# Kernel optimization log

Hardware: AMD Instinct MI355X
Metric: run time of the kernel (lower is better)

The kernel has to match this reference:

```python
import jax, jax.numpy as jnp
import numpy as np

DIM = 1024
HEADS = 16
DIM_HEAD = 64
INNER = HEADS * DIM_HEAD  # 1024
SCALE = 1.0 / DIM_HEAD ** 0.5


def setup_inputs() -> dict:
    key = jax.random.key(0)
    ks = jax.random.split(key, 5)
    x = jax.random.normal(ks[0], (4, 2048, DIM), dtype=jnp.float32)
    # nn.Linear weights stored as [out, in]; we keep [in, out] for x @ W
    Wq = jax.random.normal(ks[1], (DIM, INNER), dtype=jnp.float32) * (1.0 / np.sqrt(DIM))
    Wkv = jax.random.normal(ks[2], (DIM, 2 * INNER), dtype=jnp.float32) * (1.0 / np.sqrt(DIM))
    Wo = jax.random.normal(ks[3], (INNER, DIM), dtype=jnp.float32) * (1.0 / np.sqrt(INNER))
    bo = jax.random.normal(ks[4], (DIM,), dtype=jnp.float32) * 0.01
    return {"x": x, "Wq": Wq, "Wkv": Wkv, "Wo": Wo, "bo": bo}


def reference(x, Wq, Wkv, Wo, bo):
    b, n, _ = x.shape
    q = x @ Wq                      # [b, n, inner]
    kv = x @ Wkv                    # [b, n, 2*inner]
    k, v = jnp.split(kv, 2, axis=2)
    # 'b n (h d) -> b h n d'
    q = q.reshape(b, n, HEADS, DIM_HEAD).transpose(0, 2, 1, 3)
    k = k.reshape(b, n, HEADS, DIM_HEAD).transpose(0, 2, 1, 3)
    v = v.reshape(b, n, HEADS, DIM_HEAD).transpose(0, 2, 1, 3)
    scores = jnp.einsum('bhid,bhjd->bhij', q, k) * SCALE  # [b,h,n,n]
    attn = jax.nn.softmax(scores, axis=-1)
    out = jnp.einsum('bhij,bhjd->bhid', attn, v)          # [b,h,n,d]
    out = out.transpose(0, 2, 1, 3).reshape(b, n, INNER)  # 'b h n d -> b n (h d)'
    return out @ Wo + bo
```

## Files before the change

### kernel.cpp

```cpp
#include <hip/hip_runtime.h>
#include <hip/hip_bf16.h>

typedef unsigned short u16;
typedef unsigned int u32;
typedef __attribute__((ext_vector_type(8))) short s8v;
typedef __attribute__((ext_vector_type(4))) float f4v;
typedef __attribute__((ext_vector_type(4))) unsigned short u16x4;
typedef __attribute__((ext_vector_type(4))) unsigned int u32x4;

#define MFMA16(a,b,c) __builtin_amdgcn_mfma_f32_16x16x32_bf16((a),(b),(c),0,0,0)

#define TOKENS 8192
#define SEQ    2048
#define NH     16
#define DH     64
#define DIMK   1024
#define QPRE   0.18033688f

#if defined(__has_builtin)
#if __has_builtin(__builtin_amdgcn_exp2f)
#define EXP2(x) __builtin_amdgcn_exp2f(x)
#else
#define EXP2(x) __expf((x) * 0.69314718f)
#endif
#else
#define EXP2(x) __expf((x) * 0.69314718f)
#endif

__device__ __forceinline__ u16 f2bf(float x){
  union { float f; u32 u; } v; v.f = x;
  u32 r = v.u + 0x7FFFu + ((v.u >> 16) & 1u);
  return (u16)(r >> 16);
}

__device__ __forceinline__ void gld16(const u16* g, u16* s){
  __builtin_amdgcn_global_load_lds(
      (const __attribute__((address_space(1))) unsigned int*)(const void*)g,
      (__attribute__((address_space(3))) unsigned int*)(void*)s,
      16, 0, 0);
}

__global__ __launch_bounds__(256) void k_cast(const float* __restrict__ src,
                                              u16* __restrict__ dst){
  int i = (blockIdx.x * 256 + threadIdx.x) * 4;
  float4 v = *(const float4*)(src + i);
  u16x4 vh;
  float a[4] = {v.x, v.y, v.z, v.w};
#pragma unroll
  for (int j = 0; j < 4; j++) vh[j] = f2bf(a[j]);
  *(u16x4*)(dst + i) = vh;
}

__global__ __launch_bounds__(256) void k_transpose(const float* __restrict__ s0, int c0,
                                                   const float* __restrict__ s1, int c1,
                                                   int K, u16* __restrict__ dh){
  __shared__ float tile[64][65];
  int nb = blockIdx.x * 64, kb = blockIdx.y * 64;
  int tr = threadIdx.x >> 6, tc = threadIdx.x & 63;
#pragma unroll
  for (int i = 0; i < 16; i++){
    int k = kb + tr + i * 4, n = nb + tc;
    float v = (n < c0) ? s0[(size_t)k * c0 + n] : s1[(size_t)k * c1 + (n - c0)];
    tile[tr + i * 4][tc] = v;
  }
  __syncthreads();
#pragma unroll
  for (int i = 0; i < 16; i++){
    int nl = tr + i * 4, kl = tc;
    dh[(size_t)(nb + nl) * K + (kb + kl)] = f2bf(tile[kl][nl]);
  }
}

#define GQ_STAGE_A(buf,h,t) do{ \
  gld16(As + (size_t)(h)*131072 + (size_t)(t)*64,      &lds[(buf)*32768 + (h)*8192 + w*512]); \
  gld16(As + (size_t)(h)*131072 + (size_t)(t)*64 + 32, &lds[(buf)*32768 + (h)*8192 + 4096 + w*512]); }while(0)
#define GQ_STAGE_B(buf,h,t) do{ \
  gld16(Bs + (size_t)(h)*131072 + (size_t)(t)*64,      &lds[(buf)*32768 + 16384 + (h)*8192 + w*512]); \
  gld16(Bs + (size_t)(h)*131072 + (size_t)(t)*64 + 32, &lds[(buf)*32768 + 16384 + (h)*8192 + 4096 + w*512]); }while(0)
#define GQ_RDA(dst,buf,mh) do{ _Pragma("unroll") for (int i_ = 0; i_ < 4; i_++){ \
  dst[i_][0] = *(const s8v*)&lds[(buf)*32768 + aRB + ((mh)*4+i_)*512]; \
  dst[i_][1] = *(const s8v*)&lds[(buf)*32768 + aRB + 4096 + ((mh)*4+i_)*512]; } }while(0)
#define GQ_RDB(dst,buf,nh) do{ _Pragma("unroll") for (int j_ = 0; j_ < 2; j_++){ \
  dst[j_][0] = *(const s8v*)&lds[(buf)*32768 + bRB + ((nh)*2+j_)*512]; \
  dst[j_][1] = *(const s8v*)&lds[(buf)*32768 + bRB + 4096 + ((nh)*2+j_)*512]; } }while(0)
#define GQ_MMA(aS,bS,mh,nh) do{ __builtin_amdgcn_s_setprio(1); \
  _Pragma("unroll") for (int i_ = 0; i_ < 4; i_++) \
  _Pragma("unroll") for (int j_ = 0; j_ < 2; j_++){ \
    acc[(mh)*4+i_][(nh)*2+j_] = MFMA16(aS[i_][0], bS[j_][0], acc[(mh)*4+i_][(nh)*2+j_]); \
    acc[(mh)*4+i_][(nh)*2+j_] = MFMA16(aS[i_][1], bS[j_][1], acc[(mh)*4+i_][(nh)*2+j_]); } \
  __builtin_amdgcn_s_setprio(0); }while(0)
#define GQ_BAR() do{ asm volatile("" ::: "memory"); __builtin_amdgcn_s_barrier(); asm volatile("" ::: "memory"); }while(0)
#define GQ_VMW2() asm volatile("s_waitcnt vmcnt(2)" ::: "memory")

__global__ __launch_bounds__(512, 2) void k_gemm_qkv(
    const u16* __restrict__ A, const u16* __restrict__ B,
    u16* __restrict__ Qh, u16* __restrict__ Kh, u16* __restrict__ Vth)
{
  __shared__ u16 lds[65536];
  const int tid = threadIdx.x;
  const int w = tid >> 6, lane = tid & 63;
  const int lm = lane & 15, quad = lane >> 4;
  const int wm = w >> 2, wn = w & 3;

  const int bid = blockIdx.x;
  const int xcd = bid & 7, slot = bid >> 3;
  const int nt = slot >> 2;
  const int mloc = slot & 3;
  const int m0 = (xcd * 4 + mloc) * 256, n0 = nt * 256;

  const int srow = lane >> 2;
  const int scol = ((lane & 3) ^ (((lane >> 5) & 1) << 1)) * 8;
  const u16* As = A + (size_t)(m0 + w * 16 + srow) * DIMK + scol;
  const u16* Bs = B + (size_t)(n0 + w * 16 + srow) * DIMK + scol;

  const int swz = (lm & 8) << 1;
  const int aRB = wm * 8192 + lm * 32 + ((quad * 8) ^ swz);
  const int bRB = 16384 + (wn >> 1) * 8192 + (wn & 1) * 2048 + lm * 32 + ((quad * 8) ^ swz);

  f4v acc[8][4];
#pragma unroll
  for (int i = 0; i < 8; i++)
#pragma unroll
    for (int j = 0; j < 4; j++) acc[i][j] = (f4v){0.f, 0.f, 0.f, 0.f};

  s8v aA[4][2], aB[4][2], bA[2][2], bB[2][2];

  GQ_STAGE_A(0,0,0); GQ_STAGE_A(0,1,0); GQ_STAGE_B(0,0,0); GQ_STAGE_B(0,1,0);
  GQ_STAGE_A(1,0,1);
  GQ_VMW2(); GQ_BAR();
  GQ_RDA(aA,0,0); GQ_RDB(bA,0,0);

  for (int it = 0; it < 8; it++){
    const int t1 = 2 * it + 1;
    const int t2 = (it < 7) ? 2 * it + 2 : 15;
    const int t3 = (it < 7) ? 2 * it + 3 : 15;
    GQ_STAGE_A(1,1,t1); GQ_BAR(); GQ_RDA(aB,0,1);                 GQ_MMA(aA,bA,0,0);
    GQ_STAGE_B(1,0,t1); GQ_BAR(); GQ_RDB(bB,0,1);                 GQ_MMA(aB,bA,1,0);
    GQ_STAGE_B(1,1,t1); GQ_BAR();                                 GQ_MMA(aB,bB,1,1);
    GQ_STAGE_A(0,0,t2); GQ_VMW2(); GQ_BAR();
                                  GQ_RDA(aB,1,0); GQ_RDB(bA,1,0); GQ_MMA(aA,bB,0,1);
    GQ_STAGE_A(0,1,t2); GQ_BAR(); GQ_RDA(aA,1,1);                 GQ_MMA(aB,bA,0,0);
    GQ_STAGE_B(0,0,t2); GQ_BAR(); GQ_RDB(bB,1,1);                 GQ_MMA(aA,bA,1,0);
    GQ_STAGE_B(0,1,t2); GQ_BAR();                                 GQ_MMA(aA,bB,1,1);
    GQ_STAGE_A(1,0,t3); GQ_VMW2(); GQ_BAR();
                                  GQ_RDA(aA,0,0); GQ_RDB(bA,0,0); GQ_MMA(aB,bB,0,1);
  }

  if (nt < 8){
#pragma unroll
    for (int ig = 0; ig < 8; ig++)
#pragma unroll
      for (int jg = 0; jg < 4; jg++){
        const int gn = n0 + wn * 64 + jg * 16 + lm;
#pragma unroll
        for (int r = 0; r < 4; r++){
          const int gm = m0 + wm * 128 + ig * 16 + quad * 4 + r;
          float v = acc[ig][jg][r];
          if (gn < 1024){
            Qh[(size_t)gm * DIMK + gn] = f2bf(v * QPRE);
          } else {
            Kh[(size_t)gm * DIMK + (gn - 1024)] = f2bf(v);
          }
        }
      }
  } else {
    __syncthreads();
    u32* bnc = (u32*)lds;
#pragma unroll
    for (int igp = 0; igp < 4; igp++)
#pragma unroll
      for (int jg = 0; jg < 4; jg++){
        const int ddl = wn * 64 + jg * 16 + lm;
        const int colb = wm * 64 + igp * 16 + quad * 4;
        u32x4 p;
#pragma unroll
        for (int r = 0; r < 4; r++)
          p[r] = ((u32)f2bf(acc[2 * igp + 1][jg][r]) << 16) | (u32)f2bf(acc[2 * igp][jg][r]);
        const int col = colb ^ ((lm & 7) << 2);
        *(u32x4*)&bnc[ddl * 128 + col] = p;
      }
    __syncthreads();
    const int row = tid >> 1, half = tid & 1;
    const int df = n0 - 2048 + row;
    const int hh = df >> 6, dd = df & 63;
    const int bbat = m0 >> 11, ii0 = m0 & 2047;
    u32* Vg = (u32*)(Vth + ((size_t)(bbat * NH + hh) * DH + dd) * SEQ + ii0);
#pragma unroll
    for (int c = 0; c < 16; c++){
      const int cc = half * 16 + c;
      const int cb = (cc * 4) ^ ((row & 7) << 2);
      u32x4 q = *(const u32x4*)&bnc[row * 128 + cb];
      *(u32x4*)&Vg[cc * 4] = q;
    }
  }
}

__global__ __launch_bounds__(256) void k_gemm_op(
    const u16* __restrict__ A, const u16* __restrict__ B,
    const float* __restrict__ bias, float* __restrict__ Cf)
{
  __shared__ u16 sA[2][128*32], sB[2][128*32];
  const int tid = threadIdx.x, wave = tid >> 6, lane = tid & 63;
  const int lm = lane & 15, quad = lane >> 4;

  const int bid = blockIdx.x;
  const int xcd = bid & 7, slot = bid >> 3;
  const int nt = slot >> 3, mloc = slot & 7;
  const int m0 = (xcd * 8 + mloc) * 128, n0 = nt * 128;

  const int cof = (lane & 3) * 8;
  const int rsub = lane >> 2;

  f4v acc[4][4];
#pragma unroll
  for (int i = 0; i < 4; i++)
#pragma unroll
    for (int j = 0; j < 4; j++) acc[i][j] = (f4v){0.f, 0.f, 0.f, 0.f};

  const int wm = (wave >> 1) * 64, wn = (wave & 1) * 64;

  for (int kc = 0; kc < 16; kc++){
    int k = kc * 64;
#pragma unroll
    for (int cc = 0; cc < 2; cc++)
#pragma unroll
      for (int half = 0; half < 2; half++){
        int rb = wave * 32 + half * 16;
        gld16(A + (size_t)(m0 + rb + rsub) * DIMK + k + cc * 32 + cof, &sA[cc][rb * 32]);
        gld16(B + (size_t)(n0 + rb + rsub) * DIMK + k + cc * 32 + cof, &sB[cc][rb * 32]);
      }
    __syncthreads();

#pragma unroll
    for (int cc = 0; cc < 2; cc++){
      s8v ah[4], bh[4];
#pragma unroll
      for (int i = 0; i < 4; i++){
        ah[i] = *(const s8v*)&sA[cc][(wm + i * 16 + lm) * 32 + quad * 8];
        bh[i] = *(const s8v*)&sB[cc][(wn + i * 16 + lm) * 32 + quad * 8];
      }
#pragma unroll
      for (int i = 0; i < 4; i++)
#pragma unroll
        for (int j = 0; j < 4; j++)
          acc[i][j] = MFMA16(ah[i], bh[j], acc[i][j]);
    }
    __syncthreads();
  }

#pragma unroll
  for (int i = 0; i < 4; i++)
#pragma unroll
    for (int j = 0; j < 4; j++){
      int gn = n0 + wn + j * 16 + lm;
      float bv = bias[gn];
#pragma unroll
      for (int r = 0; r < 4; r++){
        int gm = m0 + wm + i * 16 + quad * 4 + r;
        Cf[(size_t)gm * DIMK + gn] = acc[i][j][r] + bv;
      }
    }
}

__global__ __launch_bounds__(256, 2) void k_attn(
    const u16* __restrict__ Qh, const u16* __restrict__ Kh, const u16* __restrict__ Vth,
    u16* __restrict__ Oh)
{
  __shared__ u16 sK[2*4096];
  __shared__ u16 sV[2*4096];
  __shared__ u16 sP[16384];
  u32* sPd = (u32*)sP;

  const int bid = blockIdx.x;
  const int xcd = bid & 7, slot = bid >> 3;
  const int g = xcd * 8 + (slot >> 3);
  const int qt = slot & 7;
  const int b = g >> 4, h = g & 15;

  const int tid = threadIdx.x, wave = tid >> 6, lane = tid & 63;
  const int lm = lane & 15, quad = lane >> 4;
  const int tok0 = b * SEQ + qt * 256;
  const int rsub = lane >> 2;
  const int scof = ((lane & 3) ^ (((lane >> 5) & 1) << 1)) * 8;
  const int rsw = (lm & 8) << 1;
  const int psw = (quad & 2) << 2;
  const int plm = (lm & 0xA) | ((lm & 1) << 2) | ((lm >> 2) & 1);

  s8v qf[2][4];
#pragma unroll
  for (int c = 0; c < 2; c++)
#pragma unroll
    for (int ifr = 0; ifr < 4; ifr++){
      size_t ga = (size_t)(tok0 + wave * 64 + ifr * 16 + lm) * DIMK + h * DH + c * 32 + quad * 8;
      qf[c][ifr] = *(const s8v*)(Qh + ga);
    }

  const f4v fz = (f4v){0.f, 0.f, 0.f, 0.f};

  s8v ones;
#pragma unroll
  for (int j = 0; j < 8; j++) ones[j] = (short)0x3F80;

  f4v oacc[4][4];
  f4v lacc[4];
#pragma unroll
  for (int ifr = 0; ifr < 4; ifr++){
    lacc[ifr] = (f4v){0.f, 0.f, 0.f, 0.f};
#pragma unroll
    for (int fd = 0; fd < 4; fd++) oacc[ifr][fd] = (f4v){0.f, 0.f, 0.f, 0.f};
  }

#define AT_STAGE(p, t) do{ const int jb_ = (t) * 64; \
  _Pragma("unroll") for (int c_ = 0; c_ < 2; c_++){ \
    gld16(Kh + (size_t)(b * SEQ + jb_ + wave * 16 + rsub) * DIMK + h * DH + c_ * 32 + scof, \
          &sK[(p) * 4096 + c_ * 2048 + wave * 512]); \
    gld16(Vth + (size_t)((b * NH + h) * DH + wave * 16 + rsub) * SEQ + jb_ + c_ * 32 + scof, \
          &sV[(p) * 4096 + c_ * 2048 + wave * 512]); } }while(0)
#define AT_BAR() do{ asm volatile("" ::: "memory"); __builtin_amdgcn_s_barrier(); asm volatile("" ::: "memory"); }while(0)

  AT_STAGE(0, 0);

  for (int kt = 0; kt < 32; kt++){
    const int p = kt & 1;
    AT_STAGE(p ^ 1, (kt < 31) ? (kt + 1) : 31);
    asm volatile("s_waitcnt vmcnt(4)" ::: "memory");
    AT_BAR();
    const int pb = p * 4096;

    s8v kh[2][4];
#pragma unroll
    for (int fn = 0; fn < 4; fn++){
      kh[0][fn] = *(const s8v*)&sK[pb + (fn * 16 + lm) * 32 + ((quad * 8) ^ rsw)];
      kh[1][fn] = *(const s8v*)&sK[pb + 2048 + (fn * 16 + lm) * 32 + ((quad * 8) ^ rsw)];
    }

#pragma unroll
    for (int ifr = 0; ifr < 4; ifr++){
      f4v s[4];
      __builtin_amdgcn_s_setprio(1);
#pragma unroll
      for (int fn = 0; fn < 4; fn++){
        s[fn] = MFMA16(qf[0][ifr], kh[0][fn], fz);
        s[fn] = MFMA16(qf[1][ifr], kh[1][fn], s[fn]);
      }
      __builtin_amdgcn_s_setprio(0);
#pragma unroll
      for (int fn = 0; fn < 4; fn++)
#pragma unroll
        for (int r = 0; r < 4; r++)
          s[fn][r] = EXP2(s[fn][r]);
      const int slotb = wave * 64 + ifr * 16;
#pragma unroll
      for (int r = 0; r < 4; r++){
        const int prw = slotb + (psw | ((r & 1) << 2) | (r & 2) | (quad & 1));
#pragma unroll
        for (int jc = 0; jc < 2; jc++){
          union { float f; u32 u; } a0, a1;
          a0.f = s[jc * 2 + 0][r];
          a1.f = s[jc * 2 + 1][r];
          sPd[jc * 4096 + prw * 16 + (lm ^ psw)] = __builtin_amdgcn_perm(a1.u, a0.u, 0x07060302);
        }
      }
    }

    s8v vreg[2][4];
#pragma unroll
    for (int c = 0; c < 2; c++)
#pragma unroll
      for (int fd = 0; fd < 4; fd++)
        vreg[c][fd] = *(const s8v*)&sV[pb + c * 2048 + (fd * 16 + lm) * 32 + ((quad * 8) ^ rsw)];

#pragma unroll
    for (int c = 0; c < 2; c++){
      __builtin_amdgcn_s_setprio(1);
#pragma unroll
      for (int ifr = 0; ifr < 4; ifr++){
        s8v ph = *(const s8v*)&sP[c * 8192 + (wave * 64 + ifr * 16 + plm) * 32 + ((quad * 8) ^ rsw)];
#pragma unroll
        for (int fd = 0; fd < 4; fd++)
          oacc[ifr][fd] = MFMA16(ph, vreg[c][fd], oacc[ifr][fd]);
        lacc[ifr] = MFMA16(ph, ones, lacc[ifr]);
      }
      __builtin_amdgcn_s_setprio(0);
    }
    AT_BAR();
  }

#pragma unroll
  for (int ifr = 0; ifr < 4; ifr++){
    float inv[4];
#pragma unroll
    for (int r = 0; r < 4; r++) inv[r] = 1.f / lacc[ifr][r];
#pragma unroll
    for (int fd = 0; fd < 4; fd++){
      int dcol = h * DH + fd * 16 + lm;
#pragma unroll
      for (int r = 0; r < 4; r++){
        int tok = tok0 + wave * 64 + ifr * 16 + quad * 4 + r;
        Oh[(size_t)tok * DIMK + dcol] = f2bf(oacc[ifr][fd][r] * inv[r]);
      }
    }
  }
}

extern "C" void kernel_launch(void* const* d_in, const int* in_sizes, int n_in,
                              void* d_out, int out_size, void* d_ws, size_t ws_size,
                              hipStream_t stream) {
  const float* x   = (const float*)d_in[0];
  const float* Wq  = (const float*)d_in[1];
  const float* Wkv = (const float*)d_in[2];
  const float* Wo  = (const float*)d_in[3];
  const float* bo  = (const float*)d_in[4];
  float* out = (float*)d_out;

  char* ws = (char*)d_ws;
  size_t off = 0;
  auto alloc = [&](size_t bytes) -> u16* {
    u16* p = (u16*)(ws + off);
    off += (bytes + 255) & ~(size_t)255;
    return p;
  };
  const size_t TK2 = (size_t)TOKENS * DIMK * 2;
  u16* xh  = alloc(TK2);
  u16* Wh  = alloc((size_t)3072 * DIMK * 2);
  u16* WOh = alloc((size_t)1024 * DIMK * 2);
  u16* Qh  = alloc(TK2);
  u16* Kh  = alloc(TK2);
  u16* Vth = alloc(TK2);
  u16* Oh  = alloc(TK2);

  k_cast<<<dim3((TOKENS * DIMK) / 1024), 256, 0, stream>>>(x, xh);
  k_transpose<<<dim3(48, 16), 256, 0, stream>>>(Wq, 1024, Wkv, 2048, DIMK, Wh);
  k_transpose<<<dim3(16, 16), 256, 0, stream>>>(Wo, 1024, Wo, 1024, DIMK, WOh);
  k_gemm_qkv<<<dim3(384), 512, 0, stream>>>(xh, Wh, Qh, Kh, Vth);
  k_attn<<<dim3(512), 256, 0, stream>>>(Qh, Kh, Vth, Oh);
  k_gemm_op<<<dim3(8 * 64), 256, 0, stream>>>(Oh, WOh, bo, out);
}
```

Baseline: 277.7 us.

## Keep attention P in registers via transposed S, reshape V-transpose packing, halve op GEMM tile

The attention kernel now computes S transposed (K as the A operand) so each lane's exp'd scores already sit in the B-operand layout for the PV MFMA. The scores are packed straight into registers, which removes the P round trip through LDS and its 32 KB buffer. The V-transpose epilogue in the QKV GEMM changes its packing order and swizzle to match the new P fragment layout along the key axis. The output GEMM moves to 64x128 tiles with 1024 blocks for more parallelism, at the cost of more B-tile reloads per output element.

```diff
diff --git a/kernel.cpp b/kernel.cpp
--- a/kernel.cpp
+++ b/kernel.cpp
@@ -171,11 +171,12 @@
 #pragma unroll
       for (int jg = 0; jg < 4; jg++){
         const int ddl = wn * 64 + jg * 16 + lm;
-        const int colb = wm * 64 + igp * 16 + quad * 4;
+        const int colb = (wm * 2 + (igp >> 1)) * 32 + (igp & 1) * 16 + quad * 4;
         u32x4 p;
-#pragma unroll
-        for (int r = 0; r < 4; r++)
-          p[r] = ((u32)f2bf(acc[2 * igp + 1][jg][r]) << 16) | (u32)f2bf(acc[2 * igp][jg][r]);
+        p[0] = ((u32)f2bf(acc[2 * igp][jg][1])     << 16) | (u32)f2bf(acc[2 * igp][jg][0]);
+        p[1] = ((u32)f2bf(acc[2 * igp][jg][3])     << 16) | (u32)f2bf(acc[2 * igp][jg][2]);
+        p[2] = ((u32)f2bf(acc[2 * igp + 1][jg][1]) << 16) | (u32)f2bf(acc[2 * igp + 1][jg][0]);
+        p[3] = ((u32)f2bf(acc[2 * igp + 1][jg][3]) << 16) | (u32)f2bf(acc[2 * igp + 1][jg][2]);
         const int col = colb ^ ((lm & 7) << 2);
         *(u32x4*)&bnc[ddl * 128 + col] = p;
       }
@@ -199,48 +200,49 @@
     const u16* __restrict__ A, const u16* __restrict__ B,
     const float* __restrict__ bias, float* __restrict__ Cf)
 {
-  __shared__ u16 sA[2][128*32], sB[2][128*32];
+  __shared__ u16 sA[2][64*32], sB[2][128*32];
   const int tid = threadIdx.x, wave = tid >> 6, lane = tid & 63;
   const int lm = lane & 15, quad = lane >> 4;
 
   const int bid = blockIdx.x;
   const int xcd = bid & 7, slot = bid >> 3;
-  const int nt = slot >> 3, mloc = slot & 7;
-  const int m0 = (xcd * 8 + mloc) * 128, n0 = nt * 128;
+  const int nt = slot >> 4, mloc = slot & 15;
+  const int m0 = (xcd * 16 + mloc) * 64, n0 = nt * 128;
 
   const int cof = (lane & 3) * 8;
   const int rsub = lane >> 2;
 
-  f4v acc[4][4];
-#pragma unroll
-  for (int i = 0; i < 4; i++)
+  f4v acc[2][4];
+#pragma unroll
+  for (int i = 0; i < 2; i++)
 #pragma unroll
     for (int j = 0; j < 4; j++) acc[i][j] = (f4v){0.f, 0.f, 0.f, 0.f};
 
-  const int wm = (wave >> 1) * 64, wn = (wave & 1) * 64;
+  const int wm = (wave >> 1) * 32, wn = (wave & 1) * 64;
 
   for (int kc = 0; kc < 16; kc++){
     int k = kc * 64;
 #pragma unroll
-    for (int cc = 0; cc < 2; cc++)
-#pragma unroll
-      for (int half = 0; half < 2; half++){
-        int rb = wave * 32 + half * 16;
-        gld16(A + (size_t)(m0 + rb + rsub) * DIMK + k + cc * 32 + cof, &sA[cc][rb * 32]);
-        gld16(B + (size_t)(n0 + rb + rsub) * DIMK + k + cc * 32 + cof, &sB[cc][rb * 32]);
-      }
+    for (int cc = 0; cc < 2; cc++){
+      gld16(A + (size_t)(m0 + wave * 16 + rsub) * DIMK + k + cc * 32 + cof, &sA[cc][wave * 512]);
+#pragma unroll
+      for (int h = 0; h < 2; h++)
+        gld16(B + (size_t)(n0 + h * 64 + wave * 16 + rsub) * DIMK + k + cc * 32 + cof,
+              &sB[cc][h * 2048 + wave * 512]);
+    }
     __syncthreads();
 
 #pragma unroll
     for (int cc = 0; cc < 2; cc++){
-      s8v ah[4], bh[4];
-#pragma unroll
-      for (int i = 0; i < 4; i++){
+      s8v ah[2], bh[4];
+#pragma unroll
+      for (int i = 0; i < 2; i++)
         ah[i] = *(const s8v*)&sA[cc][(wm + i * 16 + lm) * 32 + quad * 8];
-        bh[i] = *(const s8v*)&sB[cc][(wn + i * 16 + lm) * 32 + quad * 8];
-      }
-#pragma unroll
-      for (int i = 0; i < 4; i++)
+#pragma unroll
+      for (int j = 0; j < 4; j++)
+        bh[j] = *(const s8v*)&sB[cc][(wn + j * 16 + lm) * 32 + quad * 8];
+#pragma unroll
+      for (int i = 0; i < 2; i++)
 #pragma unroll
         for (int j = 0; j < 4; j++)
           acc[i][j] = MFMA16(ah[i], bh[j], acc[i][j]);
@@ -249,7 +251,7 @@
   }
 
 #pragma unroll
-  for (int i = 0; i < 4; i++)
+  for (int i = 0; i < 2; i++)
 #pragma unroll
     for (int j = 0; j < 4; j++){
       int gn = n0 + wn + j * 16 + lm;
@@ -268,8 +270,6 @@
 {
   __shared__ u16 sK[2*4096];
   __shared__ u16 sV[2*4096];
-  __shared__ u16 sP[16384];
-  u32* sPd = (u32*)sP;
 
   const int bid = blockIdx.x;
   const int xcd = bid & 7, slot = bid >> 3;
@@ -283,8 +283,6 @@
   const int rsub = lane >> 2;
   const int scof = ((lane & 3) ^ (((lane >> 5) & 1) << 1)) * 8;
   const int rsw = (lm & 8) << 1;
-  const int psw = (quad & 2) << 2;
-  const int plm = (lm & 0xA) | ((lm & 1) << 2) | ((lm >> 2) & 1);
 
   s8v qf[2][4];
 #pragma unroll
@@ -334,32 +332,34 @@
       kh[1][fn] = *(const s8v*)&sK[pb + 2048 + (fn * 16 + lm) * 32 + ((quad * 8) ^ rsw)];
     }
 
+    s8v pa[4][2];
 #pragma unroll
     for (int ifr = 0; ifr < 4; ifr++){
-      f4v s[4];
+      f4v st[4];
       __builtin_amdgcn_s_setprio(1);
 #pragma unroll
       for (int fn = 0; fn < 4; fn++){
-        s[fn] = MFMA16(qf[0][ifr], kh[0][fn], fz);
-        s[fn] = MFMA16(qf[1][ifr], kh[1][fn], s[fn]);
+        st[fn] = MFMA16(kh[0][fn], qf[0][ifr], fz);
+        st[fn] = MFMA16(kh[1][fn], qf[1][ifr], st[fn]);
       }
       __builtin_amdgcn_s_setprio(0);
 #pragma unroll
       for (int fn = 0; fn < 4; fn++)
 #pragma unroll
         for (int r = 0; r < 4; r++)
-          s[fn][r] = EXP2(s[fn][r]);
-      const int slotb = wave * 64 + ifr * 16;
-#pragma unroll
-      for (int r = 0; r < 4; r++){
-        const int prw = slotb + (psw | ((r & 1) << 2) | (r & 2) | (quad & 1));
-#pragma unroll
-        for (int jc = 0; jc < 2; jc++){
+          st[fn][r] = EXP2(st[fn][r]);
+#pragma unroll
+      for (int c = 0; c < 2; c++){
+        union { u32x4 w; s8v v; } u;
+#pragma unroll
+        for (int w2 = 0; w2 < 4; w2++){
+          const int fn = c * 2 + (w2 >> 1);
+          const int rr = (w2 & 1) * 2;
           union { float f; u32 u; } a0, a1;
-          a0.f = s[jc * 2 + 0][r];
-          a1.f = s[jc * 2 + 1][r];
-          sPd[jc * 4096 + prw * 16 + (lm ^ psw)] = __builtin_amdgcn_perm(a1.u, a0.u, 0x07060302);
+          a0.f = st[fn][rr]; a1.f = st[fn][rr + 1];
+          u.w[w2] = __builtin_amdgcn_perm(a1.u, a0.u, 0x07060302);
         }
+        pa[ifr][c] = u.v;
       }
     }
 
@@ -370,19 +370,17 @@
       for (int fd = 0; fd < 4; fd++)
         vreg[c][fd] = *(const s8v*)&sV[pb + c * 2048 + (fd * 16 + lm) * 32 + ((quad * 8) ^ rsw)];
 
-#pragma unroll
-    for (int c = 0; c < 2; c++){
-      __builtin_amdgcn_s_setprio(1);
+    __builtin_amdgcn_s_setprio(1);
+#pragma unroll
+    for (int c = 0; c < 2; c++)
 #pragma unroll
       for (int ifr = 0; ifr < 4; ifr++){
-        s8v ph = *(const s8v*)&sP[c * 8192 + (wave * 64 + ifr * 16 + plm) * 32 + ((quad * 8) ^ rsw)];
 #pragma unroll
         for (int fd = 0; fd < 4; fd++)
-          oacc[ifr][fd] = MFMA16(ph, vreg[c][fd], oacc[ifr][fd]);
-        lacc[ifr] = MFMA16(ph, ones, lacc[ifr]);
-      }
-      __builtin_amdgcn_s_setprio(0);
-    }
+          oacc[ifr][fd] = MFMA16(pa[ifr][c], vreg[c][fd], oacc[ifr][fd]);
+        lacc[ifr] = MFMA16(pa[ifr][c], ones, lacc[ifr]);
+      }
+    __builtin_amdgcn_s_setprio(0);
     AT_BAR();
   }
 
@@ -434,5 +432,5 @@
   k_transpose<<<dim3(16, 16), 256, 0, stream>>>(Wo, 1024, Wo, 1024, DIMK, WOh);
   k_gemm_qkv<<<dim3(384), 512, 0, stream>>>(xh, Wh, Qh, Kh, Vth);
   k_attn<<<dim3(512), 256, 0, stream>>>(Qh, Kh, Vth, Oh);
-  k_gemm_op<<<dim3(8 * 64), 256, 0, stream>>>(Oh, WOh, bo, out);
-}
+  k_gemm_op<<<dim3(1024), 256, 0, stream>>>(Oh, WOh, bo, out);
+}
```

Result: faster. 267.6 us (-3.6%).
